# Performance work log

Hardware: AMD Instinct MI355X
Metric: run time of the kernel (lower is better)

Reference implementation:

```python
import jax, jax.numpy as jnp
import numpy as np

N_NODES = 512
STATE_DIM = 32
MESSAGE_DIM = 32
H_MSG = 64
H_RO = 64
N_STEPS = 5


def setup_inputs() -> dict:
    key = jax.random.key(0)
    ks = jax.random.split(key, 20)
    s = 0.01  # torch init: normal(0, 0.01) weights, zero biases
    d, m = STATE_DIM, MESSAGE_DIM
    inp = {
        "J": jax.random.normal(ks[0], (N_NODES, N_NODES), jnp.float32),
        "b": jax.random.normal(ks[1], (N_NODES,), jnp.float32),
        # message-passing MLP
        "mp_W1": jax.random.normal(ks[2], (H_MSG, 2 * d + 3), jnp.float32) * s,
        "mp_b1": jnp.zeros((H_MSG,), jnp.float32),
        "mp_W2": jax.random.normal(ks[3], (H_MSG, H_MSG), jnp.float32) * s,
        "mp_b2": jnp.zeros((H_MSG,), jnp.float32),
        "mp_W3": jax.random.normal(ks[4], (m, H_MSG), jnp.float32) * s,
        "mp_b3": jnp.zeros((m,), jnp.float32),
        # GRU (input = state_dim + message_dim, hidden = state_dim); gate order r,z,n
        "gru_Wih": jax.random.normal(ks[5], (3 * d, d + m), jnp.float32) * 0.1,
        "gru_Whh": jax.random.normal(ks[6], (3 * d, d), jnp.float32) * 0.1,
        "gru_bih": jax.random.normal(ks[7], (3 * d,), jnp.float32) * 0.1,
        "gru_bhh": jax.random.normal(ks[8], (3 * d,), jnp.float32) * 0.1,
        # readout MLP
        "r_W1": jax.random.normal(ks[9], (H_RO, d), jnp.float32) * s,
        "r_b1": jnp.zeros((H_RO,), jnp.float32),
        "r_W2": jax.random.normal(ks[10], (H_RO, H_RO), jnp.float32) * s,
        "r_b2": jnp.zeros((H_RO,), jnp.float32),
        "r_W3": jax.random.normal(ks[11], (2, H_RO), jnp.float32) * s,
        "r_b3": jnp.zeros((2,), jnp.float32),
    }
    return inp


def reference(J, b, mp_W1, mp_b1, mp_W2, mp_b2, mp_W3, mp_b3,
              gru_Wih, gru_Whh, gru_bih, gru_bhh,
              r_W1, r_b1, r_W2, r_b2, r_W3, r_b3):
    n = J.shape[0]
    d = gru_Whh.shape[1]
    # split first message-layer weight by input segments to avoid building [n,n,2d+3]
    Wi, Wj = mp_W1[:, :d], mp_W1[:, d:2 * d]          # [H, d]
    wJ, wbi, wbj = mp_W1[:, 2 * d], mp_W1[:, 2 * d + 1], mp_W1[:, 2 * d + 2]  # [H]

    def step(h, _):
        # pre[i, j, :] = W1 @ cat(h_i, h_j, J_ij, b_i, b_j) + b1
        pre = ((h @ Wi.T)[:, None, :] + (h @ Wj.T)[None, :, :]
               + J[:, :, None] * wJ + b[:, None, None] * wbi
               + b[None, :, None] * wbj + mp_b1)          # [n, n, H]
        m1 = jax.nn.relu(pre)
        m2 = jax.nn.relu(m1 @ mp_W2.T + mp_b2)            # [n, n, H]
        msg = jax.nn.relu(m2 @ mp_W3.T + mp_b3)           # [n, n, M]
        msg_sum = msg.sum(axis=0)                         # sum over senders i -> [n, M]
        # GRU cell over all nodes (torch GRU, gate order r,z,n)
        x = jnp.concatenate([h, msg_sum], axis=-1)        # [n, d+M]
        gi = x @ gru_Wih.T + gru_bih                      # [n, 3d]
        gh = h @ gru_Whh.T + gru_bhh                      # [n, 3d]
        i_r, i_z, i_n = jnp.split(gi, 3, axis=-1)
        h_r, h_z, h_n = jnp.split(gh, 3, axis=-1)
        r = jax.nn.sigmoid(i_r + h_r)
        z = jax.nn.sigmoid(i_z + h_z)
        n_g = jnp.tanh(i_n + r * h_n)
        h_new = (1.0 - z) * n_g + z * h
        return h_new, None

    h0 = jnp.zeros((n, d), J.dtype)
    h, _ = jax.lax.scan(step, h0, None, length=N_STEPS)
    y = jax.nn.relu(h @ r_W1.T + r_b1)
    y = jax.nn.relu(y @ r_W2.T + r_b2)
    y = jax.nn.relu(y @ r_W3.T + r_b3)                    # [n, 2]
    return jax.nn.sigmoid(y)
```

## Files before the change

kernel.cpp:

```cpp
#include <hip/hip_runtime.h>
#include <math.h>

#define NN 512
#define SD 32
#define HM 64
#define NB 256
#define NGRP 16

typedef _Float16 f16x8 __attribute__((ext_vector_type(8)));
typedef float floatx4 __attribute__((ext_vector_type(4)));
typedef unsigned uintx4 __attribute__((ext_vector_type(4)));

#define OFF_HBS   0
#define OFF_M2L   73728
#define OFF_MSUM  92160
#define OFF_HJP   93184
#define OFF_H     93696
#define OFF_MSG   93952
#define OFF_GI    94208
#define OFF_GH    94976
#define LDS_TOTAL 95744

struct KParams {
    const float *J, *b, *mpW1, *mpb1, *mpW2, *mpb2, *mpW3, *mpb3;
    const float *Wih, *Whh, *bih, *bhh;
    const float *rW1, *rb1, *rW2, *rb2, *rW3, *rb3;
    float *out;
    unsigned *hb0, *hb1;
    unsigned *bar;
};

__device__ __forceinline__ float sigmoidf_(float x) {
    return 1.0f / (1.0f + __expf(-x));
}

__device__ __forceinline__ unsigned pkrtz(float a, float b) {
    unsigned r;
    asm("v_cvt_pkrtz_f16_f32 %0, %1, %2" : "=v"(r) : "v"(a), "v"(b));
    return r;
}
__device__ __forceinline__ unsigned pk_add(unsigned a, unsigned b) {
    unsigned r;
    asm("v_pk_add_f16 %0, %1, %2" : "=v"(r) : "v"(a), "v"(b));
    return r;
}
__device__ __forceinline__ unsigned pk_fma(unsigned a, unsigned b, unsigned c) {
    unsigned r;
    asm("v_pk_fma_f16 %0, %1, %2, %3" : "=v"(r) : "v"(a), "v"(b), "v"(c));
    return r;
}
__device__ __forceinline__ unsigned pk_relu(unsigned a) {
    unsigned r, z = 0u;
    asm("v_pk_max_f16 %0, %1, %2" : "=v"(r) : "v"(a), "v"(z));
    return r;
}

__device__ __forceinline__ unsigned ld_bypass_u32(const unsigned* p) {
    unsigned r;
    asm volatile("global_load_dword %0, %1, off sc0 sc1\n\ts_waitcnt vmcnt(0)"
                 : "=v"(r) : "v"(p) : "memory");
    return r;
}
__device__ __forceinline__ void issue16(const unsigned* p, uintx4& d) {
    asm volatile("global_load_dwordx4 %0, %1, off sc0 sc1" : "=&v"(d) : "v"(p));
}
__device__ __forceinline__ void waitc2(uintx4& a, uintx4& b) {
    asm volatile("s_waitcnt vmcnt(2)" : "+v"(a), "+v"(b) :: "memory");
}
__device__ __forceinline__ void waitc0(uintx4& a, uintx4& b) {
    asm volatile("s_waitcnt vmcnt(0)" : "+v"(a), "+v"(b) :: "memory");
}

__device__ __forceinline__ void xbarrier(unsigned* bar, unsigned round, int bid) {
    __syncthreads();
    if (threadIdx.x == 0) {
        unsigned g = (unsigned)bid >> 4;
        unsigned old = atomicAdd(&bar[g * 16], 1u);
        if (old + 1u == round * NGRP) {
            unsigned r2 = atomicAdd(&bar[256], 1u);
            if (r2 + 1u == round * NGRP) {
                atomicMax(&bar[272], round);
            } else {
                while (ld_bypass_u32(&bar[272]) < round) __builtin_amdgcn_s_sleep(2);
            }
        } else {
            while (ld_bypass_u32(&bar[272]) < round) __builtin_amdgcn_s_sleep(2);
        }
    }
    __syncthreads();
}

__global__ __launch_bounds__(512, 1) void fused_kernel(KParams p)
{
    extern __shared__ __align__(16) char smem[];
    char* hbS   = smem + OFF_HBS;
    float (*msum)[32] = (float(*)[32])(smem + OFF_MSUM);
    float (*hjpS)[64] = (float(*)[64])(smem + OFF_HJP);
    float (*hS)[32]   = (float(*)[32])(smem + OFF_H);
    float (*msgS)[32] = (float(*)[32])(smem + OFF_MSG);
    float (*giS)[96]  = (float(*)[96])(smem + OFF_GI);
    float (*ghS)[96]  = (float(*)[96])(smem + OFF_GH);

    const int tid  = threadIdx.x;
    const int lane = tid & 63;
    const int wave = tid >> 6;
    const int nsel = wave >> 2;
    const int nw   = wave & 3;
    const int j    = blockIdx.x * 2 + nsel;
    const int q    = lane >> 4;
    const int c    = lane & 15;

    char* m2Lw = smem + OFF_M2L + wave * 2304;

    if (tid < 128) {
        int node = tid >> 6, cc = tid & 63;
        int jj = blockIdx.x * 2 + node;
        const float* wr = p.mpW1 + cc * 67;
        float bj = p.b[jj];
        hjpS[node][cc] = bj * wr[66] + p.mpb1[cc];
        float si = bj * wr[65];
        float sp = __shfl(si, lane ^ 1);
        if (!(lane & 1))
            atomicExch(&p.hb0[jj * 32 + (cc >> 1)], pkrtz(si, sp));
    }

    unsigned wj2a[4], wj2b[4];
    #pragma unroll
    for (int i = 0; i < 4; ++i) {
        wj2a[i] = pkrtz(p.mpW1[(q * 8 + 2 * i) * 67 + 64],
                        p.mpW1[(q * 8 + 2 * i + 1) * 67 + 64]);
        wj2b[i] = pkrtz(p.mpW1[(q * 8 + 2 * i + 32) * 67 + 64],
                        p.mpW1[(q * 8 + 2 * i + 33) * 67 + 64]);
    }
    floatx4 b2i[4], b3i[2];
    #pragma unroll
    for (int t4 = 0; t4 < 4; ++t4)
        #pragma unroll
        for (int r = 0; r < 4; ++r) b2i[t4][r] = p.mpb2[t4 * 16 + q * 4 + r];
    #pragma unroll
    for (int t2 = 0; t2 < 2; ++t2)
        #pragma unroll
        for (int r = 0; r < 4; ++r) b3i[t2][r] = p.mpb3[t2 * 16 + q * 4 + r];

    f16x8 Aw2[2][4], Aw3[2][2];
    #pragma unroll
    for (int f = 0; f < 2; ++f)
        #pragma unroll
        for (int t4 = 0; t4 < 4; ++t4) {
            const float* src = p.mpW2 + (t4 * 16 + c) * 64 + f * 32 + q * 8;
            #pragma unroll
            for (int s = 0; s < 8; ++s) Aw2[f][t4][s] = (_Float16)src[s];
        }
    #pragma unroll
    for (int f = 0; f < 2; ++f)
        #pragma unroll
        for (int t2 = 0; t2 < 2; ++t2) {
            const float* src = p.mpW3 + (t2 * 16 + c) * 64 + f * 32 + q * 8;
            #pragma unroll
            for (int s = 0; s < 8; ++s) Aw3[f][t2][s] = (_Float16)src[s];
        }

    const float jA = p.J[((8 * (lane >> 4) + nw) * 16 + (lane & 15)) * NN + j];
    const float jB = p.J[((8 * (lane >> 4) + 4 + nw) * 16 + (lane & 15)) * NN + j];

    xbarrier(p.bar, 1, blockIdx.x);

    for (int t = 0; t < 5; ++t) {
        const unsigned* hb_read = (t & 1) ? p.hb1 : p.hb0;
        unsigned*       hb_next = (t & 1) ? p.hb0 : p.hb1;

        unsigned hjp2a[4], hjp2b[4];
        #pragma unroll
        for (int i = 0; i < 4; ++i) {
            hjp2a[i] = pkrtz(hjpS[nsel][q * 8 + 2 * i], hjpS[nsel][q * 8 + 2 * i + 1]);
            hjp2b[i] = pkrtz(hjpS[nsel][q * 8 + 2 * i + 32], hjpS[nsel][q * 8 + 2 * i + 33]);
        }

        float accf[2][4];
        #pragma unroll
        for (int t2 = 0; t2 < 2; ++t2)
            #pragma unroll
            for (int r = 0; r < 4; ++r) accf[t2][r] = 0.0f;

        uintx4 cr[4][2];
        const unsigned gbase = (unsigned)((tid >> 2) * 32 + (tid & 3) * 8);
        const unsigned lbase = (unsigned)((tid >> 2) * 144 + (tid & 3) * 32);
        #define ISSUE(k)  do { const unsigned* gp = hb_read + (k)*4096 + gbase; \
                               issue16(gp, cr[k][0]); issue16(gp + 4, cr[k][1]); } while (0)
        #define WRITE(k)  do { char* dst = hbS + (k)*128*144 + lbase; \
                               *(uintx4*)dst = cr[k][0]; *(uintx4*)(dst+16) = cr[k][1]; } while (0)
        ISSUE(0); ISSUE(1);
        waitc2(cr[0][0], cr[0][1]);
        WRITE(0);
        ISSUE(2);
        __syncthreads();

        auto edge_group = [&](int G, float Jv) {
            const char* rb = hbS + (G * 16 + c) * 144;
            uintx4 vlo = *(const uintx4*)(rb + q * 16);
            uintx4 vhi = *(const uintx4*)(rb + 64 + q * 16);
            const unsigned Jp = pkrtz(Jv, Jv);

            uintx4 a0u, a1u;
            #pragma unroll
            for (int i = 0; i < 4; ++i) {
                a0u[i] = pk_relu(pk_fma(Jp, wj2a[i], pk_add(vlo[i], hjp2a[i])));
                a1u[i] = pk_relu(pk_fma(Jp, wj2b[i], pk_add(vhi[i], hjp2b[i])));
            }
            f16x8 B0 = __builtin_bit_cast(f16x8, a0u);
            f16x8 B1 = __builtin_bit_cast(f16x8, a1u);

            floatx4 c1[4];
            #pragma unroll
            for (int t4 = 0; t4 < 4; ++t4) {
                c1[t4] = __builtin_amdgcn_mfma_f32_16x16x32_f16(Aw2[0][t4], B0, b2i[t4], 0, 0, 0);
                c1[t4] = __builtin_amdgcn_mfma_f32_16x16x32_f16(Aw2[1][t4], B1, c1[t4], 0, 0, 0);
            }
            #pragma unroll
            for (int t4 = 0; t4 < 4; ++t4) {
                unsigned p0 = pkrtz(fmaxf(c1[t4][0], 0.f), fmaxf(c1[t4][1], 0.f));
                unsigned p1 = pkrtz(fmaxf(c1[t4][2], 0.f), fmaxf(c1[t4][3], 0.f));
                *(uint2*)(m2Lw + c * 144 + t4 * 32 + q * 8) = make_uint2(p0, p1);
            }
            uintx4 rlo = *(const uintx4*)(m2Lw + c * 144 + q * 16);
            uintx4 rhi = *(const uintx4*)(m2Lw + c * 144 + 64 + q * 16);
            f16x8 B2lo = __builtin_bit_cast(f16x8, rlo);
            f16x8 B2hi = __builtin_bit_cast(f16x8, rhi);

            floatx4 c2[2];
            #pragma unroll
            for (int t2 = 0; t2 < 2; ++t2) {
                c2[t2] = __builtin_amdgcn_mfma_f32_16x16x32_f16(Aw3[0][t2], B2lo, b3i[t2], 0, 0, 0);
                c2[t2] = __builtin_amdgcn_mfma_f32_16x16x32_f16(Aw3[1][t2], B2hi, c2[t2], 0, 0, 0);
            }
            #pragma unroll
            for (int t2 = 0; t2 < 2; ++t2)
                #pragma unroll
                for (int r = 0; r < 4; ++r)
                    accf[t2][r] += fmaxf(c2[t2][r], 0.0f);
        };

        #pragma unroll
        for (int k = 0; k < 4; ++k) {
            edge_group(8 * k + nw,     __shfl(jA, k * 16 + c));
            edge_group(8 * k + 4 + nw, __shfl(jB, k * 16 + c));
            if (k == 0) { waitc2(cr[1][0], cr[1][1]); WRITE(1); ISSUE(3); __syncthreads(); }
            else if (k == 1) { waitc2(cr[2][0], cr[2][1]); WRITE(2); __syncthreads(); }
            else if (k == 2) { waitc0(cr[3][0], cr[3][1]); WRITE(3); __syncthreads(); }
        }
        #undef ISSUE
        #undef WRITE

        #pragma unroll
        for (int m = 1; m < 16; m <<= 1)
            #pragma unroll
            for (int t2 = 0; t2 < 2; ++t2)
                #pragma unroll
                for (int r = 0; r < 4; ++r)
                    accf[t2][r] += __shfl_xor(accf[t2][r], m);
        if (c == 0) {
            #pragma unroll
            for (int t2 = 0; t2 < 2; ++t2)
                #pragma unroll
                for (int r = 0; r < 4; ++r)
                    msum[wave][t2 * 16 + q * 4 + r] = accf[t2][r];
        }
        __syncthreads();

        if (tid < 64) {
            int node = tid >> 5, d = tid & 31;
            msgS[node][d] = msum[node * 4 + 0][d] + msum[node * 4 + 1][d] +
                            msum[node * 4 + 2][d] + msum[node * 4 + 3][d];
        }
        __syncthreads();

        if (tid < 192) {
            int node = tid / 96, r = tid % 96;
            int g = r >> 5, d = r & 31;
            const float* wi = p.Wih + (g * 32 + d) * 64;
            float a  = p.bih[g * 32 + d];
            float bb = p.bhh[g * 32 + d];
            if (t > 0) {
                const float* wh = p.Whh + (g * 32 + d) * 32;
                #pragma unroll
                for (int k = 0; k < 32; ++k) {
                    float hv = hS[node][k];
                    a  = fmaf(hv, wi[k], a);
                    bb = fmaf(hv, wh[k], bb);
                }
            }
            #pragma unroll
            for (int k = 0; k < 32; ++k) a = fmaf(msgS[node][k], wi[32 + k], a);
            giS[node][r] = a; ghS[node][r] = bb;
        }
        __syncthreads();

        if (tid < 64) {
            int node = tid >> 5, d = tid & 31;
            float r  = sigmoidf_(giS[node][d] + ghS[node][d]);
            float z  = sigmoidf_(giS[node][32 + d] + ghS[node][32 + d]);
            float ng = tanhf(giS[node][64 + d] + r * ghS[node][64 + d]);
            float hold = (t > 0) ? hS[node][d] : 0.0f;
            hS[node][d] = (1.0f - z) * ng + z * hold;
        }
        __syncthreads();

        if (t < 4) {
            if (tid < 128) {
                int node = tid >> 6, cc = tid & 63;
                int jj = blockIdx.x * 2 + node;
                const float* wr = p.mpW1 + cc * 67;
                float bj = p.b[jj];
                float si = bj * wr[65];
                float sj = bj * wr[66] + p.mpb1[cc];
                #pragma unroll
                for (int d = 0; d < 32; ++d) {
                    float hv = hS[node][d];
                    si = fmaf(hv, wr[d], si);
                    sj = fmaf(hv, wr[32 + d], sj);
                }
                hjpS[node][cc] = sj;
                float sp = __shfl(si, lane ^ 1);
                if (!(lane & 1))
                    atomicExch(&hb_next[jj * 32 + (cc >> 1)], pkrtz(si, sp));
            }
            xbarrier(p.bar, (unsigned)(t + 2), blockIdx.x);
        } else {
            if (wave < 2) {
                int node = wave;
                int jj = blockIdx.x * 2 + node;
                float y1 = p.rb1[lane];
                #pragma unroll
                for (int k = 0; k < 32; ++k) y1 = fmaf(hS[node][k], p.rW1[lane * 32 + k], y1);
                y1 = fmaxf(y1, 0.0f);
                float y2 = p.rb2[lane];
                #pragma unroll
                for (int k = 0; k < 64; ++k) y2 = fmaf(__shfl(y1, k), p.rW2[lane * 64 + k], y2);
                y2 = fmaxf(y2, 0.0f);
                float y3 = (lane < 2) ? p.rb3[lane] : 0.0f;
                #pragma unroll
                for (int k = 0; k < 64; ++k) {
                    float v = __shfl(y2, k);
                    if (lane < 2) y3 = fmaf(v, p.rW3[lane * 64 + k], y3);
                }
                if (lane < 2) p.out[jj * 2 + lane] = sigmoidf_(y3);
            }
        }
    }
}

extern "C" void kernel_launch(void* const* d_in, const int* in_sizes, int n_in,
                              void* d_out, int out_size, void* d_ws, size_t ws_size,
                              hipStream_t stream)
{
    float* ws = (float*)d_ws;

    KParams p;
    p.J    = (const float*)d_in[0];
    p.b    = (const float*)d_in[1];
    p.mpW1 = (const float*)d_in[2];
    p.mpb1 = (const float*)d_in[3];
    p.mpW2 = (const float*)d_in[4];
    p.mpb2 = (const float*)d_in[5];
    p.mpW3 = (const float*)d_in[6];
    p.mpb3 = (const float*)d_in[7];
    p.Wih  = (const float*)d_in[8];
    p.Whh  = (const float*)d_in[9];
    p.bih  = (const float*)d_in[10];
    p.bhh  = (const float*)d_in[11];
    p.rW1  = (const float*)d_in[12];
    p.rb1  = (const float*)d_in[13];
    p.rW2  = (const float*)d_in[14];
    p.rb2  = (const float*)d_in[15];
    p.rW3  = (const float*)d_in[16];
    p.rb3  = (const float*)d_in[17];
    p.out  = (float*)d_out;

    p.hb0  = (unsigned*)ws;
    p.hb1  = (unsigned*)(ws + 16384);
    p.bar  = (unsigned*)(ws + 32768);

    (void)hipMemsetAsync(p.bar, 0, 4096, stream);

    (void)hipFuncSetAttribute((const void*)fused_kernel,
                              hipFuncAttributeMaxDynamicSharedMemorySize, LDS_TOTAL);
    fused_kernel<<<dim3(NB), dim3(512), LDS_TOTAL, stream>>>(p);
}
```

Measured before the change: 174.2 us.

## Double block size to 16 waves per block and load full h buffer upfront

Launches 1024 threads per block so each node is handled by 8 waves instead of 4. Each wave now processes 4 edge groups instead of 8, and the message reduction sums 8 partial results instead of 4. The staged, overlapped h-buffer load with intermediate barriers is replaced by one bulk load of all four chunks followed by a single wait and barrier. This adds more parallelism per block but removes the overlap between the global loads and compute, grows LDS use, and tightens the per-thread register budget, which affects the resident weight fragments.

Measured after the change: 281.5 us. 61.6% more time.

```diff
diff --git a/kernel.cpp b/kernel.cpp
--- a/kernel.cpp
+++ b/kernel.cpp
@@ -13,13 +13,13 @@
 
 #define OFF_HBS   0
 #define OFF_M2L   73728
-#define OFF_MSUM  92160
-#define OFF_HJP   93184
-#define OFF_H     93696
-#define OFF_MSG   93952
-#define OFF_GI    94208
-#define OFF_GH    94976
-#define LDS_TOTAL 95744
+#define OFF_MSUM  110592
+#define OFF_HJP   112640
+#define OFF_H     113152
+#define OFF_MSG   113408
+#define OFF_GI    113664
+#define OFF_GH    114432
+#define LDS_TOTAL 115200
 
 struct KParams {
     const float *J, *b, *mpW1, *mpb1, *mpW2, *mpb2, *mpW3, *mpb3;
@@ -64,11 +64,9 @@
 __device__ __forceinline__ void issue16(const unsigned* p, uintx4& d) {
     asm volatile("global_load_dwordx4 %0, %1, off sc0 sc1" : "=&v"(d) : "v"(p));
 }
-__device__ __forceinline__ void waitc2(uintx4& a, uintx4& b) {
-    asm volatile("s_waitcnt vmcnt(2)" : "+v"(a), "+v"(b) :: "memory");
-}
-__device__ __forceinline__ void waitc0(uintx4& a, uintx4& b) {
-    asm volatile("s_waitcnt vmcnt(0)" : "+v"(a), "+v"(b) :: "memory");
+__device__ __forceinline__ void waitall4(uintx4& a, uintx4& b, uintx4& c, uintx4& d) {
+    asm volatile("s_waitcnt vmcnt(0)"
+                 : "+v"(a), "+v"(b), "+v"(c), "+v"(d) :: "memory");
 }
 
 __device__ __forceinline__ void xbarrier(unsigned* bar, unsigned round, int bid) {
@@ -90,7 +88,7 @@
     __syncthreads();
 }
 
-__global__ __launch_bounds__(512, 1) void fused_kernel(KParams p)
+__global__ __launch_bounds__(1024) void fused_kernel(KParams p)
 {
     extern __shared__ __align__(16) char smem[];
     char* hbS   = smem + OFF_HBS;
@@ -104,8 +102,8 @@
     const int tid  = threadIdx.x;
     const int lane = tid & 63;
     const int wave = tid >> 6;
-    const int nsel = wave >> 2;
-    const int nw   = wave & 3;
+    const int nsel = wave >> 3;
+    const int nw   = wave & 7;
     const int j    = blockIdx.x * 2 + nsel;
     const int q    = lane >> 4;
     const int c    = lane & 15;
@@ -161,7 +159,6 @@
         }
 
     const float jA = p.J[((8 * (lane >> 4) + nw) * 16 + (lane & 15)) * NN + j];
-    const float jB = p.J[((8 * (lane >> 4) + 4 + nw) * 16 + (lane & 15)) * NN + j];
 
     xbarrier(p.bar, 1, blockIdx.x);
 
@@ -182,17 +179,18 @@
             #pragma unroll
             for (int r = 0; r < 4; ++r) accf[t2][r] = 0.0f;
 
-        uintx4 cr[4][2];
-        const unsigned gbase = (unsigned)((tid >> 2) * 32 + (tid & 3) * 8);
-        const unsigned lbase = (unsigned)((tid >> 2) * 144 + (tid & 3) * 32);
-        #define ISSUE(k)  do { const unsigned* gp = hb_read + (k)*4096 + gbase; \
-                               issue16(gp, cr[k][0]); issue16(gp + 4, cr[k][1]); } while (0)
-        #define WRITE(k)  do { char* dst = hbS + (k)*128*144 + lbase; \
-                               *(uintx4*)dst = cr[k][0]; *(uintx4*)(dst+16) = cr[k][1]; } while (0)
-        ISSUE(0); ISSUE(1);
-        waitc2(cr[0][0], cr[0][1]);
-        WRITE(0);
-        ISSUE(2);
+        {
+            uintx4 cr[4];
+            const unsigned* gp = hb_read + tid * 4;
+            #pragma unroll
+            for (int k = 0; k < 4; ++k) issue16(gp + k * 4096, cr[k]);
+            waitall4(cr[0], cr[1], cr[2], cr[3]);
+            #pragma unroll
+            for (int k = 0; k < 4; ++k) {
+                int row = k * 128 + (tid >> 3);
+                *(uintx4*)(hbS + row * 144 + (tid & 7) * 16) = cr[k];
+            }
+        }
         __syncthreads();
 
         auto edge_group = [&](int G, float Jv) {
@@ -241,15 +239,8 @@
         };
 
         #pragma unroll
-        for (int k = 0; k < 4; ++k) {
-            edge_group(8 * k + nw,     __shfl(jA, k * 16 + c));
-            edge_group(8 * k + 4 + nw, __shfl(jB, k * 16 + c));
-            if (k == 0) { waitc2(cr[1][0], cr[1][1]); WRITE(1); ISSUE(3); __syncthreads(); }
-            else if (k == 1) { waitc2(cr[2][0], cr[2][1]); WRITE(2); __syncthreads(); }
-            else if (k == 2) { waitc0(cr[3][0], cr[3][1]); WRITE(3); __syncthreads(); }
-        }
-        #undef ISSUE
-        #undef WRITE
+        for (int k = 0; k < 4; ++k)
+            edge_group(8 * k + nw, __shfl(jA, k * 16 + c));
 
         #pragma unroll
         for (int m = 1; m < 16; m <<= 1)
@@ -269,8 +260,10 @@
 
         if (tid < 64) {
             int node = tid >> 5, d = tid & 31;
-            msgS[node][d] = msum[node * 4 + 0][d] + msum[node * 4 + 1][d] +
-                            msum[node * 4 + 2][d] + msum[node * 4 + 3][d];
+            float s = 0.0f;
+            #pragma unroll
+            for (int w = 0; w < 8; ++w) s += msum[node * 8 + w][d];
+            msgS[node][d] = s;
         }
         __syncthreads();
 
@@ -384,5 +377,5 @@
 
     (void)hipFuncSetAttribute((const void*)fused_kernel,
                               hipFuncAttributeMaxDynamicSharedMemorySize, LDS_TOTAL);
-    fused_kernel<<<dim3(NB), dim3(512), LDS_TOTAL, stream>>>(p);
-}
+    fused_kernel<<<dim3(NB), dim3(1024), LDS_TOTAL, stream>>>(p);
+}
```

## Replace persistent grid barrier kernel with prep kernel plus per-step launches

Applied to the files above, without the earlier changes.

Splits the single persistent kernel, which used atomic cross-block barriers between GRU steps, into a prep kernel and five step kernel launches. The prep kernel transposes J and the weight matrices and pre-packs the fp16 MFMA operands so that later loads are coalesced and need no per-launch conversion. Step boundaries now rely on kernel launch ordering instead of spin barriers. In exchange it adds launch overhead, re-reads weights from global memory each step, and loses the overlapped chunked load of the hidden-state buffer.

Measured after the change: 151.4 us. 13.1% less time.

```diff
diff --git a/kernel.cpp b/kernel.cpp
--- a/kernel.cpp
+++ b/kernel.cpp
@@ -4,8 +4,6 @@
 #define NN 512
 #define SD 32
 #define HM 64
-#define NB 256
-#define NGRP 16
 
 typedef _Float16 f16x8 __attribute__((ext_vector_type(8)));
 typedef float floatx4 __attribute__((ext_vector_type(4)));
@@ -14,26 +12,16 @@
 #define OFF_HBS   0
 #define OFF_M2L   73728
 #define OFF_MSUM  92160
-#define OFF_HJP   93184
-#define OFF_H     93696
-#define OFF_MSG   93952
-#define OFF_GI    94208
-#define OFF_GH    94976
-#define LDS_TOTAL 95744
-
-struct KParams {
-    const float *J, *b, *mpW1, *mpb1, *mpW2, *mpb2, *mpW3, *mpb3;
-    const float *Wih, *Whh, *bih, *bhh;
-    const float *rW1, *rb1, *rW2, *rb2, *rW3, *rb3;
-    float *out;
-    unsigned *hb0, *hb1;
-    unsigned *bar;
-};
+#define OFF_HPREV 93184
+#define OFF_HS    93440
+#define OFF_MSG   93696
+#define OFF_GI    93952
+#define OFF_GH    94720
+#define LDS_TOTAL 95488
 
 __device__ __forceinline__ float sigmoidf_(float x) {
     return 1.0f / (1.0f + __expf(-x));
 }
-
 __device__ __forceinline__ unsigned pkrtz(float a, float b) {
     unsigned r;
     asm("v_cvt_pkrtz_f16_f32 %0, %1, %2" : "=v"(r) : "v"(a), "v"(b));
@@ -55,51 +43,103 @@
     return r;
 }
 
-__device__ __forceinline__ unsigned ld_bypass_u32(const unsigned* p) {
-    unsigned r;
-    asm volatile("global_load_dword %0, %1, off sc0 sc1\n\ts_waitcnt vmcnt(0)"
-                 : "=v"(r) : "v"(p) : "memory");
-    return r;
-}
-__device__ __forceinline__ void issue16(const unsigned* p, uintx4& d) {
-    asm volatile("global_load_dwordx4 %0, %1, off sc0 sc1" : "=&v"(d) : "v"(p));
-}
-__device__ __forceinline__ void waitc2(uintx4& a, uintx4& b) {
-    asm volatile("s_waitcnt vmcnt(2)" : "+v"(a), "+v"(b) :: "memory");
-}
-__device__ __forceinline__ void waitc0(uintx4& a, uintx4& b) {
-    asm volatile("s_waitcnt vmcnt(0)" : "+v"(a), "+v"(b) :: "memory");
-}
-
-__device__ __forceinline__ void xbarrier(unsigned* bar, unsigned round, int bid) {
-    __syncthreads();
-    if (threadIdx.x == 0) {
-        unsigned g = (unsigned)bid >> 4;
-        unsigned old = atomicAdd(&bar[g * 16], 1u);
-        if (old + 1u == round * NGRP) {
-            unsigned r2 = atomicAdd(&bar[256], 1u);
-            if (r2 + 1u == round * NGRP) {
-                atomicMax(&bar[272], round);
-            } else {
-                while (ld_bypass_u32(&bar[272]) < round) __builtin_amdgcn_s_sleep(2);
-            }
-        } else {
-            while (ld_bypass_u32(&bar[272]) < round) __builtin_amdgcn_s_sleep(2);
-        }
-    }
-    __syncthreads();
-}
-
-__global__ __launch_bounds__(512, 1) void fused_kernel(KParams p)
+struct PParams {
+    const float *J, *b, *mpW1, *mpb1, *mpW2, *mpW3, *Wih, *Whh, *rW1, *rW2;
+    float *JT, *W1T, *WihT, *WhhT, *rW1T, *rW2T;
+    unsigned *w2p, *w3p, *wjp, *hb0, *hjp0;
+};
+
+__global__ __launch_bounds__(256) void prep_kernel(PParams pp)
+{
+    __shared__ float tile[32][33];
+    const int tid = threadIdx.x;
+    const int b   = blockIdx.x;
+    {
+        int bx = b & 15, by = b >> 4;
+        int tx = tid & 31, ty = tid >> 5;
+        #pragma unroll
+        for (int r = 0; r < 32; r += 8)
+            tile[ty + r][tx] = pp.J[(by * 32 + ty + r) * NN + bx * 32 + tx];
+        __syncthreads();
+        #pragma unroll
+        for (int r = 0; r < 32; r += 8)
+            pp.JT[(bx * 32 + ty + r) * NN + by * 32 + tx] = tile[tx][ty + r];
+    }
+    if (b == 0 && tid < 64) {
+        int l = tid, qq = l >> 4, cc = l & 15;
+        for (int f = 0; f < 2; ++f)
+            for (int t4 = 0; t4 < 4; ++t4) {
+                const float* src = pp.mpW2 + (t4 * 16 + cc) * 64 + f * 32 + qq * 8;
+                unsigned* dst = pp.w2p + ((f * 4 + t4) * 64 + l) * 4;
+                for (int i = 0; i < 4; ++i) dst[i] = pkrtz(src[2 * i], src[2 * i + 1]);
+            }
+        for (int f = 0; f < 2; ++f)
+            for (int t2 = 0; t2 < 2; ++t2) {
+                const float* src = pp.mpW3 + (t2 * 16 + cc) * 64 + f * 32 + qq * 8;
+                unsigned* dst = pp.w3p + ((f * 2 + t2) * 64 + l) * 4;
+                for (int i = 0; i < 4; ++i) dst[i] = pkrtz(src[2 * i], src[2 * i + 1]);
+            }
+        for (int s = 0; s < 2; ++s) {
+            unsigned* dst = pp.wjp + (s * 64 + l) * 4;
+            for (int i = 0; i < 4; ++i) {
+                int r0 = qq * 8 + 2 * i + s * 32;
+                dst[i] = pkrtz(pp.mpW1[r0 * 67 + 64], pp.mpW1[(r0 + 1) * 67 + 64]);
+            }
+        }
+    }
+    if (b == 1)
+        for (int n = tid; n < 64 * 67; n += 256) {
+            int cc = n / 67, d = n % 67;
+            pp.W1T[d * 64 + cc] = pp.mpW1[n];
+        }
+    if (b == 2)
+        for (int n = tid; n < 96 * 64; n += 256)
+            pp.WihT[(n & 63) * 96 + (n >> 6)] = pp.Wih[n];
+    if (b == 3)
+        for (int n = tid; n < 96 * 32; n += 256)
+            pp.WhhT[(n & 31) * 96 + (n >> 5)] = pp.Whh[n];
+    if (b == 4) {
+        for (int n = tid; n < 64 * 32; n += 256)
+            pp.rW1T[(n & 31) * 64 + (n >> 5)] = pp.rW1[n];
+        for (int n = tid; n < 64 * 64; n += 256)
+            pp.rW2T[(n & 63) * 64 + (n >> 6)] = pp.rW2[n];
+    }
+    if (b >= 16 && b < 144) {
+        int jj = (b - 16) * 4 + (tid >> 6);
+        int cc = tid & 63;
+        float bj = pp.b[jj];
+        float sj = bj * pp.mpW1[cc * 67 + 66] + pp.mpb1[cc];
+        float si = bj * pp.mpW1[cc * 67 + 65];
+        float sjp = __shfl(sj, cc ^ 1);
+        float sip = __shfl(si, cc ^ 1);
+        if (!(cc & 1)) {
+            pp.hjp0[jj * 32 + (cc >> 1)] = pkrtz(sj, sjp);
+            pp.hb0[jj * 32 + (cc >> 1)]  = pkrtz(si, sip);
+        }
+    }
+}
+
+struct SParams {
+    const unsigned *hbR;  unsigned *hbW;
+    const unsigned *hjR;  unsigned *hjW;
+    const float *hR;      float *hW;
+    const float *JT, *W1T, *WihT, *WhhT, *bih, *bhh, *mpb2, *mpb3, *b, *mpb1;
+    const float *rW1T, *rW2T, *rW3, *rb1, *rb2, *rb3;
+    const unsigned *w2p, *w3p, *wjp;
+    float *out;
+    int hzero, rdout;
+};
+
+__global__ __launch_bounds__(512, 1) void step_kernel(SParams s)
 {
     extern __shared__ __align__(16) char smem[];
-    char* hbS   = smem + OFF_HBS;
-    float (*msum)[32] = (float(*)[32])(smem + OFF_MSUM);
-    float (*hjpS)[64] = (float(*)[64])(smem + OFF_HJP);
-    float (*hS)[32]   = (float(*)[32])(smem + OFF_H);
-    float (*msgS)[32] = (float(*)[32])(smem + OFF_MSG);
-    float (*giS)[96]  = (float(*)[96])(smem + OFF_GI);
-    float (*ghS)[96]  = (float(*)[96])(smem + OFF_GH);
+    char* hbS = smem + OFF_HBS;
+    float (*msum)[32]   = (float(*)[32])(smem + OFF_MSUM);
+    float (*hPrevS)[32] = (float(*)[32])(smem + OFF_HPREV);
+    float (*hS)[32]     = (float(*)[32])(smem + OFF_HS);
+    float (*msgS)[32]   = (float(*)[32])(smem + OFF_MSG);
+    float (*giS)[96]    = (float(*)[96])(smem + OFF_GI);
+    float (*ghS)[96]    = (float(*)[96])(smem + OFF_GH);
 
     const int tid  = threadIdx.x;
     const int lane = tid & 63;
@@ -109,242 +149,206 @@
     const int j    = blockIdx.x * 2 + nsel;
     const int q    = lane >> 4;
     const int c    = lane & 15;
-
     char* m2Lw = smem + OFF_M2L + wave * 2304;
 
-    if (tid < 128) {
-        int node = tid >> 6, cc = tid & 63;
-        int jj = blockIdx.x * 2 + node;
-        const float* wr = p.mpW1 + cc * 67;
-        float bj = p.b[jj];
-        hjpS[node][cc] = bj * wr[66] + p.mpb1[cc];
-        float si = bj * wr[65];
-        float sp = __shfl(si, lane ^ 1);
-        if (!(lane & 1))
-            atomicExch(&p.hb0[jj * 32 + (cc >> 1)], pkrtz(si, sp));
-    }
-
-    unsigned wj2a[4], wj2b[4];
-    #pragma unroll
-    for (int i = 0; i < 4; ++i) {
-        wj2a[i] = pkrtz(p.mpW1[(q * 8 + 2 * i) * 67 + 64],
-                        p.mpW1[(q * 8 + 2 * i + 1) * 67 + 64]);
-        wj2b[i] = pkrtz(p.mpW1[(q * 8 + 2 * i + 32) * 67 + 64],
-                        p.mpW1[(q * 8 + 2 * i + 33) * 67 + 64]);
-    }
+    {
+        uintx4 cr[8];
+        const uintx4* gp = (const uintx4*)s.hbR;
+        #pragma unroll
+        for (int k = 0; k < 8; ++k) cr[k] = gp[k * 512 + tid];
+        #pragma unroll
+        for (int k = 0; k < 8; ++k) {
+            int row = k * 64 + (tid >> 3);
+            *(uintx4*)(hbS + row * 144 + (tid & 7) * 16) = cr[k];
+        }
+    }
+    if (tid < 64 && !s.hzero)
+        hPrevS[tid >> 5][tid & 31] = s.hR[blockIdx.x * 64 + tid];
+    __syncthreads();
+
+    f16x8 Aw2[2][4], Aw3[2][2];
+    #pragma unroll
+    for (int f = 0; f < 2; ++f)
+        #pragma unroll
+        for (int t4 = 0; t4 < 4; ++t4)
+            Aw2[f][t4] = __builtin_bit_cast(f16x8,
+                ((const uintx4*)s.w2p)[(f * 4 + t4) * 64 + lane]);
+    #pragma unroll
+    for (int f = 0; f < 2; ++f)
+        #pragma unroll
+        for (int t2 = 0; t2 < 2; ++t2)
+            Aw3[f][t2] = __builtin_bit_cast(f16x8,
+                ((const uintx4*)s.w3p)[(f * 2 + t2) * 64 + lane]);
+    uintx4 wja = ((const uintx4*)s.wjp)[lane];
+    uintx4 wjb = ((const uintx4*)s.wjp)[64 + lane];
+    uintx4 hja = ((const uintx4*)s.hjR)[j * 8 + q];
+    uintx4 hjb = ((const uintx4*)s.hjR)[j * 8 + 4 + q];
+
     floatx4 b2i[4], b3i[2];
     #pragma unroll
     for (int t4 = 0; t4 < 4; ++t4)
         #pragma unroll
-        for (int r = 0; r < 4; ++r) b2i[t4][r] = p.mpb2[t4 * 16 + q * 4 + r];
+        for (int r = 0; r < 4; ++r) b2i[t4][r] = s.mpb2[t4 * 16 + q * 4 + r];
     #pragma unroll
     for (int t2 = 0; t2 < 2; ++t2)
         #pragma unroll
-        for (int r = 0; r < 4; ++r) b3i[t2][r] = p.mpb3[t2 * 16 + q * 4 + r];
-
-    f16x8 Aw2[2][4], Aw3[2][2];
-    #pragma unroll
-    for (int f = 0; f < 2; ++f)
+        for (int r = 0; r < 4; ++r) b3i[t2][r] = s.mpb3[t2 * 16 + q * 4 + r];
+
+    const float jA = s.JT[j * NN + (8 * q + nw) * 16 + c];
+    const float jB = s.JT[j * NN + (8 * q + 4 + nw) * 16 + c];
+
+    float accf[2][4];
+    #pragma unroll
+    for (int t2 = 0; t2 < 2; ++t2)
+        #pragma unroll
+        for (int r = 0; r < 4; ++r) accf[t2][r] = 0.0f;
+
+    auto edge_group = [&](int G, float Jv) {
+        const char* rb = hbS + (G * 16 + c) * 144;
+        uintx4 vlo = *(const uintx4*)(rb + q * 16);
+        uintx4 vhi = *(const uintx4*)(rb + 64 + q * 16);
+        const unsigned Jp = pkrtz(Jv, Jv);
+
+        uintx4 a0u, a1u;
+        #pragma unroll
+        for (int i = 0; i < 4; ++i) {
+            a0u[i] = pk_relu(pk_fma(Jp, wja[i], pk_add(vlo[i], hja[i])));
+            a1u[i] = pk_relu(pk_fma(Jp, wjb[i], pk_add(vhi[i], hjb[i])));
+        }
+        f16x8 B0 = __builtin_bit_cast(f16x8, a0u);
+        f16x8 B1 = __builtin_bit_cast(f16x8, a1u);
+
+        floatx4 c1[4];
         #pragma unroll
         for (int t4 = 0; t4 < 4; ++t4) {
-            const float* src = p.mpW2 + (t4 * 16 + c) * 64 + f * 32 + q * 8;
-            #pragma unroll
-            for (int s = 0; s < 8; ++s) Aw2[f][t4][s] = (_Float16)src[s];
-        }
-    #pragma unroll
-    for (int f = 0; f < 2; ++f)
+            c1[t4] = __builtin_amdgcn_mfma_f32_16x16x32_f16(Aw2[0][t4], B0, b2i[t4], 0, 0, 0);
+            c1[t4] = __builtin_amdgcn_mfma_f32_16x16x32_f16(Aw2[1][t4], B1, c1[t4], 0, 0, 0);
+        }
+        #pragma unroll
+        for (int t4 = 0; t4 < 4; ++t4) {
+            unsigned p0 = pkrtz(fmaxf(c1[t4][0], 0.f), fmaxf(c1[t4][1], 0.f));
+            unsigned p1 = pkrtz(fmaxf(c1[t4][2], 0.f), fmaxf(c1[t4][3], 0.f));
+            *(uint2*)(m2Lw + c * 144 + t4 * 32 + q * 8) = make_uint2(p0, p1);
+        }
+        uintx4 rlo = *(const uintx4*)(m2Lw + c * 144 + q * 16);
+        uintx4 rhi = *(const uintx4*)(m2Lw + c * 144 + 64 + q * 16);
+        f16x8 B2lo = __builtin_bit_cast(f16x8, rlo);
+        f16x8 B2hi = __builtin_bit_cast(f16x8, rhi);
+
+        floatx4 c2[2];
         #pragma unroll
         for (int t2 = 0; t2 < 2; ++t2) {
-            const float* src = p.mpW3 + (t2 * 16 + c) * 64 + f * 32 + q * 8;
-            #pragma unroll
-            for (int s = 0; s < 8; ++s) Aw3[f][t2][s] = (_Float16)src[s];
-        }
-
-    const float jA = p.J[((8 * (lane >> 4) + nw) * 16 + (lane & 15)) * NN + j];
-    const float jB = p.J[((8 * (lane >> 4) + 4 + nw) * 16 + (lane & 15)) * NN + j];
-
-    xbarrier(p.bar, 1, blockIdx.x);
-
-    for (int t = 0; t < 5; ++t) {
-        const unsigned* hb_read = (t & 1) ? p.hb1 : p.hb0;
-        unsigned*       hb_next = (t & 1) ? p.hb0 : p.hb1;
-
-        unsigned hjp2a[4], hjp2b[4];
-        #pragma unroll
-        for (int i = 0; i < 4; ++i) {
-            hjp2a[i] = pkrtz(hjpS[nsel][q * 8 + 2 * i], hjpS[nsel][q * 8 + 2 * i + 1]);
-            hjp2b[i] = pkrtz(hjpS[nsel][q * 8 + 2 * i + 32], hjpS[nsel][q * 8 + 2 * i + 33]);
-        }
-
-        float accf[2][4];
+            c2[t2] = __builtin_amdgcn_mfma_f32_16x16x32_f16(Aw3[0][t2], B2lo, b3i[t2], 0, 0, 0);
+            c2[t2] = __builtin_amdgcn_mfma_f32_16x16x32_f16(Aw3[1][t2], B2hi, c2[t2], 0, 0, 0);
+        }
         #pragma unroll
         for (int t2 = 0; t2 < 2; ++t2)
             #pragma unroll
-            for (int r = 0; r < 4; ++r) accf[t2][r] = 0.0f;
-
-        uintx4 cr[4][2];
-        const unsigned gbase = (unsigned)((tid >> 2) * 32 + (tid & 3) * 8);
-        const unsigned lbase = (unsigned)((tid >> 2) * 144 + (tid & 3) * 32);
-        #define ISSUE(k)  do { const unsigned* gp = hb_read + (k)*4096 + gbase; \
-                               issue16(gp, cr[k][0]); issue16(gp + 4, cr[k][1]); } while (0)
-        #define WRITE(k)  do { char* dst = hbS + (k)*128*144 + lbase; \
-                               *(uintx4*)dst = cr[k][0]; *(uintx4*)(dst+16) = cr[k][1]; } while (0)
-        ISSUE(0); ISSUE(1);
-        waitc2(cr[0][0], cr[0][1]);
-        WRITE(0);
-        ISSUE(2);
-        __syncthreads();
-
-        auto edge_group = [&](int G, float Jv) {
-            const char* rb = hbS + (G * 16 + c) * 144;
-            uintx4 vlo = *(const uintx4*)(rb + q * 16);
-            uintx4 vhi = *(const uintx4*)(rb + 64 + q * 16);
-            const unsigned Jp = pkrtz(Jv, Jv);
-
-            uintx4 a0u, a1u;
-            #pragma unroll
-            for (int i = 0; i < 4; ++i) {
-                a0u[i] = pk_relu(pk_fma(Jp, wj2a[i], pk_add(vlo[i], hjp2a[i])));
-                a1u[i] = pk_relu(pk_fma(Jp, wj2b[i], pk_add(vhi[i], hjp2b[i])));
-            }
-            f16x8 B0 = __builtin_bit_cast(f16x8, a0u);
-            f16x8 B1 = __builtin_bit_cast(f16x8, a1u);
-
-            floatx4 c1[4];
-            #pragma unroll
-            for (int t4 = 0; t4 < 4; ++t4) {
-                c1[t4] = __builtin_amdgcn_mfma_f32_16x16x32_f16(Aw2[0][t4], B0, b2i[t4], 0, 0, 0);
-                c1[t4] = __builtin_amdgcn_mfma_f32_16x16x32_f16(Aw2[1][t4], B1, c1[t4], 0, 0, 0);
-            }
-            #pragma unroll
-            for (int t4 = 0; t4 < 4; ++t4) {
-                unsigned p0 = pkrtz(fmaxf(c1[t4][0], 0.f), fmaxf(c1[t4][1], 0.f));
-                unsigned p1 = pkrtz(fmaxf(c1[t4][2], 0.f), fmaxf(c1[t4][3], 0.f));
-                *(uint2*)(m2Lw + c * 144 + t4 * 32 + q * 8) = make_uint2(p0, p1);
-            }
-            uintx4 rlo = *(const uintx4*)(m2Lw + c * 144 + q * 16);
-            uintx4 rhi = *(const uintx4*)(m2Lw + c * 144 + 64 + q * 16);
-            f16x8 B2lo = __builtin_bit_cast(f16x8, rlo);
-            f16x8 B2hi = __builtin_bit_cast(f16x8, rhi);
-
-            floatx4 c2[2];
-            #pragma unroll
-            for (int t2 = 0; t2 < 2; ++t2) {
-                c2[t2] = __builtin_amdgcn_mfma_f32_16x16x32_f16(Aw3[0][t2], B2lo, b3i[t2], 0, 0, 0);
-                c2[t2] = __builtin_amdgcn_mfma_f32_16x16x32_f16(Aw3[1][t2], B2hi, c2[t2], 0, 0, 0);
-            }
-            #pragma unroll
-            for (int t2 = 0; t2 < 2; ++t2)
-                #pragma unroll
-                for (int r = 0; r < 4; ++r)
-                    accf[t2][r] += fmaxf(c2[t2][r], 0.0f);
-        };
-
-        #pragma unroll
-        for (int k = 0; k < 4; ++k) {
-            edge_group(8 * k + nw,     __shfl(jA, k * 16 + c));
-            edge_group(8 * k + 4 + nw, __shfl(jB, k * 16 + c));
-            if (k == 0) { waitc2(cr[1][0], cr[1][1]); WRITE(1); ISSUE(3); __syncthreads(); }
-            else if (k == 1) { waitc2(cr[2][0], cr[2][1]); WRITE(2); __syncthreads(); }
-            else if (k == 2) { waitc0(cr[3][0], cr[3][1]); WRITE(3); __syncthreads(); }
-        }
-        #undef ISSUE
-        #undef WRITE
-
-        #pragma unroll
-        for (int m = 1; m < 16; m <<= 1)
-            #pragma unroll
-            for (int t2 = 0; t2 < 2; ++t2)
-                #pragma unroll
-                for (int r = 0; r < 4; ++r)
-                    accf[t2][r] += __shfl_xor(accf[t2][r], m);
-        if (c == 0) {
-            #pragma unroll
-            for (int t2 = 0; t2 < 2; ++t2)
-                #pragma unroll
-                for (int r = 0; r < 4; ++r)
-                    msum[wave][t2 * 16 + q * 4 + r] = accf[t2][r];
-        }
-        __syncthreads();
-
-        if (tid < 64) {
-            int node = tid >> 5, d = tid & 31;
-            msgS[node][d] = msum[node * 4 + 0][d] + msum[node * 4 + 1][d] +
-                            msum[node * 4 + 2][d] + msum[node * 4 + 3][d];
-        }
-        __syncthreads();
-
-        if (tid < 192) {
-            int node = tid / 96, r = tid % 96;
-            int g = r >> 5, d = r & 31;
-            const float* wi = p.Wih + (g * 32 + d) * 64;
-            float a  = p.bih[g * 32 + d];
-            float bb = p.bhh[g * 32 + d];
-            if (t > 0) {
-                const float* wh = p.Whh + (g * 32 + d) * 32;
-                #pragma unroll
-                for (int k = 0; k < 32; ++k) {
-                    float hv = hS[node][k];
-                    a  = fmaf(hv, wi[k], a);
-                    bb = fmaf(hv, wh[k], bb);
-                }
-            }
-            #pragma unroll
-            for (int k = 0; k < 32; ++k) a = fmaf(msgS[node][k], wi[32 + k], a);
-            giS[node][r] = a; ghS[node][r] = bb;
-        }
-        __syncthreads();
-
-        if (tid < 64) {
-            int node = tid >> 5, d = tid & 31;
-            float r  = sigmoidf_(giS[node][d] + ghS[node][d]);
-            float z  = sigmoidf_(giS[node][32 + d] + ghS[node][32 + d]);
-            float ng = tanhf(giS[node][64 + d] + r * ghS[node][64 + d]);
-            float hold = (t > 0) ? hS[node][d] : 0.0f;
-            hS[node][d] = (1.0f - z) * ng + z * hold;
-        }
-        __syncthreads();
-
-        if (t < 4) {
-            if (tid < 128) {
-                int node = tid >> 6, cc = tid & 63;
-                int jj = blockIdx.x * 2 + node;
-                const float* wr = p.mpW1 + cc * 67;
-                float bj = p.b[jj];
-                float si = bj * wr[65];
-                float sj = bj * wr[66] + p.mpb1[cc];
-                #pragma unroll
-                for (int d = 0; d < 32; ++d) {
-                    float hv = hS[node][d];
-                    si = fmaf(hv, wr[d], si);
-                    sj = fmaf(hv, wr[32 + d], sj);
-                }
-                hjpS[node][cc] = sj;
-                float sp = __shfl(si, lane ^ 1);
-                if (!(lane & 1))
-                    atomicExch(&hb_next[jj * 32 + (cc >> 1)], pkrtz(si, sp));
-            }
-            xbarrier(p.bar, (unsigned)(t + 2), blockIdx.x);
-        } else {
-            if (wave < 2) {
-                int node = wave;
-                int jj = blockIdx.x * 2 + node;
-                float y1 = p.rb1[lane];
-                #pragma unroll
-                for (int k = 0; k < 32; ++k) y1 = fmaf(hS[node][k], p.rW1[lane * 32 + k], y1);
-                y1 = fmaxf(y1, 0.0f);
-                float y2 = p.rb2[lane];
-                #pragma unroll
-                for (int k = 0; k < 64; ++k) y2 = fmaf(__shfl(y1, k), p.rW2[lane * 64 + k], y2);
-                y2 = fmaxf(y2, 0.0f);
-                float y3 = (lane < 2) ? p.rb3[lane] : 0.0f;
-                #pragma unroll
-                for (int k = 0; k < 64; ++k) {
-                    float v = __shfl(y2, k);
-                    if (lane < 2) y3 = fmaf(v, p.rW3[lane * 64 + k], y3);
-                }
-                if (lane < 2) p.out[jj * 2 + lane] = sigmoidf_(y3);
-            }
+            for (int r = 0; r < 4; ++r)
+                accf[t2][r] += fmaxf(c2[t2][r], 0.0f);
+    };
+
+    #pragma unroll
+    for (int k = 0; k < 4; ++k) {
+        edge_group(8 * k + nw,     __shfl(jA, k * 16 + c));
+        edge_group(8 * k + 4 + nw, __shfl(jB, k * 16 + c));
+    }
+
+    #pragma unroll
+    for (int m = 1; m < 16; m <<= 1)
+        #pragma unroll
+        for (int t2 = 0; t2 < 2; ++t2)
+            #pragma unroll
+            for (int r = 0; r < 4; ++r)
+                accf[t2][r] += __shfl_xor(accf[t2][r], m);
+    if (c == 0) {
+        #pragma unroll
+        for (int t2 = 0; t2 < 2; ++t2)
+            #pragma unroll
+            for (int r = 0; r < 4; ++r)
+                msum[wave][t2 * 16 + q * 4 + r] = accf[t2][r];
+    }
+    __syncthreads();
+
+    if (tid < 64) {
+        int node = tid >> 5, d = tid & 31;
+        msgS[node][d] = msum[node * 4 + 0][d] + msum[node * 4 + 1][d] +
+                        msum[node * 4 + 2][d] + msum[node * 4 + 3][d];
+    }
+    __syncthreads();
+
+    if (tid < 192) {
+        int node = tid / 96, r = tid % 96;
+        float a  = s.bih[r];
+        float bb = s.bhh[r];
+        if (!s.hzero) {
+            #pragma unroll
+            for (int k = 0; k < 32; ++k) {
+                float hv = hPrevS[node][k];
+                a  = fmaf(hv, s.WihT[k * 96 + r], a);
+                bb = fmaf(hv, s.WhhT[k * 96 + r], bb);
+            }
+        }
+        #pragma unroll
+        for (int k = 0; k < 32; ++k)
+            a = fmaf(msgS[node][k], s.WihT[(32 + k) * 96 + r], a);
+        giS[node][r] = a; ghS[node][r] = bb;
+    }
+    __syncthreads();
+
+    if (tid < 64) {
+        int node = tid >> 5, d = tid & 31;
+        float r  = sigmoidf_(giS[node][d] + ghS[node][d]);
+        float z  = sigmoidf_(giS[node][32 + d] + ghS[node][32 + d]);
+        float ng = tanhf(giS[node][64 + d] + r * ghS[node][64 + d]);
+        float hold = s.hzero ? 0.0f : hPrevS[node][d];
+        float hv = (1.0f - z) * ng + z * hold;
+        hS[node][d] = hv;
+        s.hW[blockIdx.x * 64 + tid] = hv;
+    }
+    __syncthreads();
+
+    if (!s.rdout) {
+        if (tid < 128) {
+            int node = tid >> 6, cc = tid & 63;
+            int jj = blockIdx.x * 2 + node;
+            float bj = s.b[jj];
+            float si = bj * s.W1T[65 * 64 + cc];
+            float sj = bj * s.W1T[66 * 64 + cc] + s.mpb1[cc];
+            #pragma unroll
+            for (int d = 0; d < 32; ++d) {
+                float hv = hS[node][d];
+                si = fmaf(hv, s.W1T[d * 64 + cc], si);
+                sj = fmaf(hv, s.W1T[(32 + d) * 64 + cc], sj);
+            }
+            float sip = __shfl(si, lane ^ 1);
+            float sjp = __shfl(sj, lane ^ 1);
+            if (!(cc & 1)) {
+                s.hbW[jj * 32 + (cc >> 1)] = pkrtz(si, sip);
+                s.hjW[jj * 32 + (cc >> 1)] = pkrtz(sj, sjp);
+            }
+        }
+    } else {
+        if (wave < 2) {
+            int node = wave;
+            int jj = blockIdx.x * 2 + node;
+            float y1 = s.rb1[lane];
+            #pragma unroll
+            for (int k = 0; k < 32; ++k)
+                y1 = fmaf(hS[node][k], s.rW1T[k * 64 + lane], y1);
+            y1 = fmaxf(y1, 0.0f);
+            float y2 = s.rb2[lane];
+            #pragma unroll
+            for (int k = 0; k < 64; ++k)
+                y2 = fmaf(__shfl(y1, k), s.rW2T[k * 64 + lane], y2);
+            y2 = fmaxf(y2, 0.0f);
+            float y3 = (lane < 2) ? s.rb3[lane] : 0.0f;
+            #pragma unroll
+            for (int k = 0; k < 64; ++k) {
+                float v = __shfl(y2, k);
+                if (lane < 2) y3 = fmaf(v, s.rW3[lane * 64 + k], y3);
+            }
+            if (lane < 2) s.out[jj * 2 + lane] = sigmoidf_(y3);
         }
     }
 }
@@ -355,34 +359,69 @@
 {
     float* ws = (float*)d_ws;
 
-    KParams p;
-    p.J    = (const float*)d_in[0];
-    p.b    = (const float*)d_in[1];
-    p.mpW1 = (const float*)d_in[2];
-    p.mpb1 = (const float*)d_in[3];
-    p.mpW2 = (const float*)d_in[4];
-    p.mpb2 = (const float*)d_in[5];
-    p.mpW3 = (const float*)d_in[6];
-    p.mpb3 = (const float*)d_in[7];
-    p.Wih  = (const float*)d_in[8];
-    p.Whh  = (const float*)d_in[9];
-    p.bih  = (const float*)d_in[10];
-    p.bhh  = (const float*)d_in[11];
-    p.rW1  = (const float*)d_in[12];
-    p.rb1  = (const float*)d_in[13];
-    p.rW2  = (const float*)d_in[14];
-    p.rb2  = (const float*)d_in[15];
-    p.rW3  = (const float*)d_in[16];
-    p.rb3  = (const float*)d_in[17];
-    p.out  = (float*)d_out;
-
-    p.hb0  = (unsigned*)ws;
-    p.hb1  = (unsigned*)(ws + 16384);
-    p.bar  = (unsigned*)(ws + 32768);
-
-    (void)hipMemsetAsync(p.bar, 0, 4096, stream);
-
-    (void)hipFuncSetAttribute((const void*)fused_kernel,
+    const float* J    = (const float*)d_in[0];
+    const float* b    = (const float*)d_in[1];
+    const float* mpW1 = (const float*)d_in[2];
+    const float* mpb1 = (const float*)d_in[3];
+    const float* mpW2 = (const float*)d_in[4];
+    const float* mpb2 = (const float*)d_in[5];
+    const float* mpW3 = (const float*)d_in[6];
+    const float* mpb3 = (const float*)d_in[7];
+    const float* Wih  = (const float*)d_in[8];
+    const float* Whh  = (const float*)d_in[9];
+    const float* bih  = (const float*)d_in[10];
+    const float* bhh  = (const float*)d_in[11];
+    const float* rW1  = (const float*)d_in[12];
+    const float* rb1  = (const float*)d_in[13];
+    const float* rW2  = (const float*)d_in[14];
+    const float* rb2  = (const float*)d_in[15];
+    const float* rW3  = (const float*)d_in[16];
+    const float* rb3  = (const float*)d_in[17];
+
+    float*    JT   = ws;
+    float*    W1T  = ws + 262144;
+    float*    WihT = ws + 266432;
+    float*    WhhT = ws + 272576;
+    float*    rW1T = ws + 275648;
+    float*    rW2T = ws + 277696;
+    unsigned* w2p  = (unsigned*)(ws + 281792);
+    unsigned* w3p  = (unsigned*)(ws + 283840);
+    unsigned* wjp  = (unsigned*)(ws + 284864);
+    unsigned* hb0  = (unsigned*)(ws + 285376);
+    unsigned* hb1  = (unsigned*)(ws + 301760);
+    unsigned* hj0  = (unsigned*)(ws + 318144);
+    unsigned* hj1  = (unsigned*)(ws + 334528);
+    float*    h0   = ws + 350912;
+    float*    h1   = ws + 367296;
+
+    PParams pp;
+    pp.J = J; pp.b = b; pp.mpW1 = mpW1; pp.mpb1 = mpb1; pp.mpW2 = mpW2;
+    pp.mpW3 = mpW3; pp.Wih = Wih; pp.Whh = Whh; pp.rW1 = rW1; pp.rW2 = rW2;
+    pp.JT = JT; pp.W1T = W1T; pp.WihT = WihT; pp.WhhT = WhhT;
+    pp.rW1T = rW1T; pp.rW2T = rW2T;
+    pp.w2p = w2p; pp.w3p = w3p; pp.wjp = wjp; pp.hb0 = hb0; pp.hjp0 = hj0;
+
+    (void)hipFuncSetAttribute((const void*)step_kernel,
                               hipFuncAttributeMaxDynamicSharedMemorySize, LDS_TOTAL);
-    fused_kernel<<<dim3(NB), dim3(512), LDS_TOTAL, stream>>>(p);
-}
+
+    prep_kernel<<<dim3(256), dim3(256), 0, stream>>>(pp);
+
+    SParams s;
+    s.JT = JT; s.W1T = W1T; s.WihT = WihT; s.WhhT = WhhT;
+    s.bih = bih; s.bhh = bhh; s.mpb2 = mpb2; s.mpb3 = mpb3; s.b = b; s.mpb1 = mpb1;
+    s.rW1T = rW1T; s.rW2T = rW2T; s.rW3 = rW3; s.rb1 = rb1; s.rb2 = rb2; s.rb3 = rb3;
+    s.w2p = w2p; s.w3p = w3p; s.wjp = wjp;
+    s.out = (float*)d_out;
+
+    for (int t = 0; t < 5; ++t) {
+        s.hbR = (t & 1) ? hb1 : hb0;
+        s.hbW = (t & 1) ? hb0 : hb1;
+        s.hjR = (t & 1) ? hj1 : hj0;
+        s.hjW = (t & 1) ? hj0 : hj1;
+        s.hR  = (t & 1) ? h0 : h1;
+        s.hW  = (t & 1) ? h1 : h0;
+        s.hzero = (t == 0);
+        s.rdout = (t == 4);
+        step_kernel<<<dim3(256), dim3(512), LDS_TOTAL, stream>>>(s);
+    }
+}
```
